# Kernel optimization log

Measured on AMD Instinct MI355X. Metric: run time of the kernel, lower is better.

The kernel has to match this reference:

```python
import jax, jax.numpy as jnp
import numpy as np

H = 12     # attention heads
W1S = 256  # one-sided sliding window (attention_window = 512)
NW = 8     # n_windows -> global tokens at each window start


def ln(x, g, b, eps=1e-5):
    m = jnp.mean(x, -1, keepdims=True)
    v = jnp.mean(jnp.square(x - m), -1, keepdims=True)
    return (x - m) * jax.lax.rsqrt(v + eps) * g + b


def _forward(x, x_mask, word_emb, pos_emb, emb_g, emb_b, Wq, bq, Wk, bk, Wv, bv, Wo, bo,
             Wqg, bqg, Wkg, bkg, Wvg, bvg, ln1_g, ln1_b, W1, b1, W2, b2, ln2_g, ln2_b,
             out_w, out_b):
    B, S = x.shape
    D = word_emb.shape[1]
    Dh = D // H
    w = W1S
    nb = S // w
    win_len = S // NW
    g = NW
    gpos = jnp.arange(g) * win_len
    scale = 1.0 / np.sqrt(Dh)

    x_mask = x_mask.at[:, gpos].set(1)  # module forces global slots to be valid
    kmask = x_mask > 0
    is_glob = jnp.zeros((S,), bool).at[gpos].set(True)

    h = ln(word_emb[x] + pos_emb[None], emb_g, emb_b)

    # static masks for the banded (sliding-window) scores
    kidx = jnp.arange(nb)[:, None] * w + jnp.arange(3 * w)[None, :] - w  # [nb,3w] abs key idx
    in_rng = (kidx >= 0) & (kidx < S)
    kidx_c = jnp.clip(kidx, 0, S - 1)
    key_ok = in_rng[None] & kmask[:, kidx_c] & (~is_glob[kidx_c])[None]   # [B,nb,3w]
    diff = jnp.arange(3 * w)[None, :] - w - jnp.arange(w)[:, None]        # [w,3w] key-query offset
    band_mask = ((jnp.abs(diff) <= w)[None, None] & key_ok[:, :, None, :]).reshape(B, 1, S, 3 * w)
    gkey_mask = kmask[:, gpos][:, None, None, :]                           # [B,1,1,g]
    mask_all = jnp.concatenate([jnp.broadcast_to(gkey_mask, (B, 1, S, g)),
                                jnp.broadcast_to(band_mask, (B, 1, S, 3 * w))], -1)

    def heads(t):
        return t.reshape(B, S, H, Dh).transpose(0, 2, 1, 3)

    def chunk3(t):  # [B,H,S,Dh] -> [B,H,nb,3w,Dh]; block n covers key offsets [-w, 2w)
        tp = jnp.pad(t, ((0, 0), (0, 0), (w, w), (0, 0))).reshape(B, H, nb + 2, w, Dh)
        return jnp.concatenate([tp[:, :, :nb], tp[:, :, 1:nb + 1], tp[:, :, 2:]], axis=3)

    def layer(h, p):
        (wq, bq_, wk, bk_, wv, bv_, wo, bo_, wqg, bqg_, wkg, bkg_, wvg, bvg_,
         g1, gb1, w1, fb1, w2, fb2, g2, gb2) = p
        q = heads(h @ wq + bq_); k = heads(h @ wk + bk_); v = heads(h @ wv + bv_)
        # sliding-window band scores + extra global-key columns, joint softmax
        sb = jnp.einsum('bhnqd,bhnkd->bhnqk', q.reshape(B, H, nb, w, Dh), chunk3(k)) * scale
        sg = jnp.einsum('bhsd,bhgd->bhsg', q, k[:, :, gpos]) * scale
        scores = jnp.concatenate([sg, sb.reshape(B, H, S, 3 * w)], -1)
        neg = jnp.finfo(scores.dtype).min * 0.5
        probs = jax.nn.softmax(jnp.where(mask_all, scores, neg), -1)
        ctx = (jnp.einsum('bhnqk,bhnkd->bhnqd', probs[..., g:].reshape(B, H, nb, w, 3 * w), chunk3(v)).reshape(B, H, S, Dh)
               + jnp.einsum('bhsg,bhgd->bhsd', probs[..., :g], v[:, :, gpos]))
        ctx = ctx.transpose(0, 2, 1, 3).reshape(B, S, D)
        # global-token queries: full attention over all keys with separate projections
        qg = (h[:, gpos] @ wqg + bqg_).reshape(B, g, H, Dh).transpose(0, 2, 1, 3)
        kg = heads(h @ wkg + bkg_); vg = heads(h @ wvg + bvg_)
        sgl = jnp.where(kmask[:, None, None, :], jnp.einsum('bhgd,bhsd->bhgs', qg, kg) * scale, neg)
        ctxg = jnp.einsum('bhgs,bhsd->bhgd', jax.nn.softmax(sgl, -1), vg).transpose(0, 2, 1, 3).reshape(B, g, D)
        ctx = ctx.at[:, gpos].set(ctxg)
        h = ln(h + ctx @ wo + bo_, g1, gb1)
        h = ln(h + jax.nn.gelu(h @ w1 + fb1, approximate=False) @ w2 + fb2, g2, gb2)
        return h, None

    params = (Wq, bq, Wk, bk, Wv, bv, Wo, bo, Wqg, bqg, Wkg, bkg, Wvg, bvg,
              ln1_g, ln1_b, W1, b1, W2, b2, ln2_g, ln2_b)
    h, _ = jax.lax.scan(jax.checkpoint(layer), h, params)
    y = h.reshape(B * NW, win_len, D)[:, 0]   # CLS pooling per window
    return y @ out_w + out_b


def setup_inputs():
    key = jax.random.key(0)
    V, S, D, L, F, O, B = 50265, 4096, 768, 12, 3072, 128, 1
    ks = iter(jax.random.split(key, 40))
    def nrm(shape):
        return (jax.random.normal(next(ks), shape) * 0.02).astype(jnp.float32)
    inp = {
        'x': jax.random.randint(next(ks), (B, S), 0, V, dtype=jnp.int32),
        'x_mask': jnp.ones((B, S), jnp.int32),
        'word_emb': nrm((V, D)), 'pos_emb': nrm((S, D)),
        'emb_g': jnp.ones((D,)), 'emb_b': jnp.zeros((D,)),
        'Wq': nrm((L, D, D)), 'bq': jnp.zeros((L, D)),
        'Wk': nrm((L, D, D)), 'bk': jnp.zeros((L, D)),
        'Wv': nrm((L, D, D)), 'bv': jnp.zeros((L, D)),
        'Wo': nrm((L, D, D)), 'bo': jnp.zeros((L, D)),
        'Wqg': nrm((L, D, D)), 'bqg': jnp.zeros((L, D)),
        'Wkg': nrm((L, D, D)), 'bkg': jnp.zeros((L, D)),
        'Wvg': nrm((L, D, D)), 'bvg': jnp.zeros((L, D)),
        'ln1_g': jnp.ones((L, D)), 'ln1_b': jnp.zeros((L, D)),
        'W1': nrm((L, D, F)), 'b1': jnp.zeros((L, F)),
        'W2': nrm((L, F, D)), 'b2': jnp.zeros((L, D)),
        'ln2_g': jnp.ones((L, D)), 'ln2_b': jnp.zeros((L, D)),
        'out_w': nrm((D, O)), 'out_b': jnp.zeros((O,)),
    }
    return inp


def reference(x, x_mask, word_emb, pos_emb, emb_g, emb_b, Wq, bq, Wk, bk, Wv, bv, Wo, bo,
              Wqg, bqg, Wkg, bkg, Wvg, bvg, ln1_g, ln1_b, W1, b1, W2, b2, ln2_g, ln2_b,
              out_w, out_b):
    return _forward(x, x_mask, word_emb, pos_emb, emb_g, emb_b, Wq, bq, Wk, bk, Wv, bv,
                    Wo, bo, Wqg, bqg, Wkg, bkg, Wvg, bvg, ln1_g, ln1_b, W1, b1, W2, b2,
                    ln2_g, ln2_b, out_w, out_b)
```

## Files before the change

### kernel.cpp

```cpp
#include <hip/hip_runtime.h>
#include <cstddef>

#define S_LEN   4096
#define DMODEL  768
#define NHEAD   12
#define DHEAD   64
#define FDIM    3072
#define NLAYER  12
#define WIN     256
#define NGLOB   8
#define GSTRIDE 512

typedef short bf16x8 __attribute__((ext_vector_type(8)));
typedef float f32x4 __attribute__((ext_vector_type(4)));
typedef unsigned short u16;

__device__ __forceinline__ u16 f2bf(float f) {
  unsigned u = __builtin_bit_cast(unsigned, f);
  return (u16)((u + 0x7FFFu + ((u >> 16) & 1u)) >> 16);
}
__device__ __forceinline__ float bf2f(u16 s) {
  unsigned u = ((unsigned)s) << 16;
  return __builtin_bit_cast(float, u);
}

__device__ __forceinline__ void gload16(const void* g, void* l) {
  __builtin_amdgcn_global_load_lds(
      (const __attribute__((address_space(1))) void*)g,
      (__attribute__((address_space(3))) void*)l, 16, 0, 0);
}

__device__ __forceinline__ float wave_sum(float v) {
#pragma unroll
  for (int off = 32; off > 0; off >>= 1) v += __shfl_xor(v, off);
  return v;
}

__device__ __forceinline__ float block_sum256(float v, float* sbuf) {
  v = wave_sum(v);
  int w = threadIdx.x >> 6;
  __syncthreads();
  if ((threadIdx.x & 63) == 0) sbuf[w] = v;
  __syncthreads();
  return sbuf[0] + sbuf[1] + sbuf[2] + sbuf[3];
}

__global__ __launch_bounds__(256) void embed_ln_kernel(
    const int* __restrict__ x, const float* __restrict__ wemb,
    const float* __restrict__ pemb, const float* __restrict__ gg,
    const float* __restrict__ bb, float* __restrict__ h, u16* __restrict__ hb) {
  __shared__ float sbuf[4];
  int s = blockIdx.x, tid = threadIdx.x;
  int idx = x[s];
  float vals[3];
#pragma unroll
  for (int i = 0; i < 3; i++) {
    int d = tid + i * 256;
    vals[i] = wemb[(size_t)idx * DMODEL + d] + pemb[(size_t)s * DMODEL + d];
  }
  float mean = block_sum256(vals[0] + vals[1] + vals[2], sbuf) * (1.0f / 768.0f);
  float sq = 0.f;
#pragma unroll
  for (int i = 0; i < 3; i++) { float t = vals[i] - mean; sq += t * t; }
  float inv = rsqrtf(block_sum256(sq, sbuf) * (1.0f / 768.0f) + 1e-5f);
#pragma unroll
  for (int i = 0; i < 3; i++) {
    int d = tid + i * 256;
    float r = (vals[i] - mean) * inv * gg[d] + bb[d];
    h[(size_t)s * DMODEL + d] = r;
    hb[(size_t)s * DMODEL + d] = f2bf(r);
  }
}

__global__ __launch_bounds__(256) void add_ln_kernel(
    float* __restrict__ h, const float* __restrict__ r,
    const float* __restrict__ gg, const float* __restrict__ bb,
    u16* __restrict__ hb) {
  __shared__ float sbuf[4];
  int s = blockIdx.x, tid = threadIdx.x;
  float vals[3];
#pragma unroll
  for (int i = 0; i < 3; i++) {
    int d = tid + i * 256;
    vals[i] = h[(size_t)s * DMODEL + d] + r[(size_t)s * DMODEL + d];
  }
  float mean = block_sum256(vals[0] + vals[1] + vals[2], sbuf) * (1.0f / 768.0f);
  float sq = 0.f;
#pragma unroll
  for (int i = 0; i < 3; i++) { float t = vals[i] - mean; sq += t * t; }
  float inv = rsqrtf(block_sum256(sq, sbuf) * (1.0f / 768.0f) + 1e-5f);
#pragma unroll
  for (int i = 0; i < 3; i++) {
    int d = tid + i * 256;
    float rr = (vals[i] - mean) * inv * gg[d] + bb[d];
    h[(size_t)s * DMODEL + d] = rr;
    hb[(size_t)s * DMODEL + d] = f2bf(rr);
  }
}

#define DD_ ((size_t)DMODEL * DMODEL)
#define DF_ ((size_t)DMODEL * FDIM)
#define WSTRIDE (6 * DD_ + 2 * DF_)
__global__ __launch_bounds__(256) void convw_kernel(
    const float* __restrict__ Wq, const float* __restrict__ Wk,
    const float* __restrict__ Wv, const float* __restrict__ Wkg,
    const float* __restrict__ Wvg, const float* __restrict__ Wo,
    const float* __restrict__ W1, const float* __restrict__ W2,
    u16* __restrict__ wt) {
  int l = blockIdx.y;
  int bid = blockIdx.x;
  const float* src; u16* dst; int K, N, r;
  u16* base = wt + (size_t)l * WSTRIDE;
  if (bid < 864) {
    int m = bid / 144; r = bid % 144; K = 768; N = 768;
    switch (m) {
      case 0: src = Wq  + l * DD_; dst = base;           break;
      case 1: src = Wk  + l * DD_; dst = base + 1 * DD_; break;
      case 2: src = Wv  + l * DD_; dst = base + 2 * DD_; break;
      case 3: src = Wkg + l * DD_; dst = base + 3 * DD_; break;
      case 4: src = Wvg + l * DD_; dst = base + 4 * DD_; break;
      default: src = Wo + l * DD_; dst = base + 5 * DD_; break;
    }
  } else if (bid < 1440) {
    r = bid - 864; K = 768; N = 3072; src = W1 + l * DF_; dst = base + 6 * DD_;
  } else {
    r = bid - 1440; K = 3072; N = 768; src = W2 + l * DF_; dst = base + 6 * DD_ + DF_;
  }
  int nt = N / 64;
  int tk = (r / nt) * 64, tn = (r % nt) * 64;
  int t = threadIdx.x;
  int c = t >> 2, ko = t & 3;
#pragma unroll
  for (int p = 0; p < 2; p++) {
    int kb = (p * 4 + ko) * 8;
    const float* sp = src + (size_t)(tk + kb) * N + tn + c;
    bf16x8 val;
#pragma unroll
    for (int j = 0; j < 8; j++) val[j] = (short)f2bf(sp[(size_t)j * N]);
    *(bf16x8*)&dst[(size_t)(tn + c) * K + tk + kb] = val;
  }
}

template <int ACT, int OUTM, int TM>
__device__ __forceinline__ void mm_core(const u16* __restrict__ A, const u16* __restrict__ Wt,
                                        const float* __restrict__ bias, void* __restrict__ Cv,
                                        int M, int N, int K, int bm, int bn,
                                        u16* As, u16* Bs) {
  constexpr int MR = TM / 32;
  constexpr int AJ = TM / 32;
  int t = threadIdx.x;
  int wid = t >> 6, lane = t & 63;
  int wr = (wid >> 1) * (TM / 2), wc = (wid & 1) * 64;
  int lr = lane & 15, lg = lane >> 4;
  f32x4 acc[MR][4];
  f32x4 zf = {0.f, 0.f, 0.f, 0.f};
#pragma unroll
  for (int m = 0; m < MR; m++)
#pragma unroll
    for (int n = 0; n < 4; n++) acc[m][n] = zf;

  int srow = wid * 8 + (lane >> 3);
  int sgr = (lane & 7) ^ (lane >> 3);
  const u16* aSrc = A + (size_t)(bm + srow) * K + sgr * 8;
  const u16* bSrc = Wt + (size_t)(bn + srow) * K + sgr * 8;
  int dstOff = wid * 8 * 64;

  for (int kt = 0; kt < K; kt += 64) {
    __syncthreads();
#pragma unroll
    for (int j = 0; j < AJ; j++)
      gload16(aSrc + kt + (size_t)j * 32 * K, As + dstOff + j * 32 * 64);
#pragma unroll
    for (int j = 0; j < 4; j++)
      gload16(bSrc + kt + (size_t)j * 32 * K, Bs + dstOff + j * 32 * 64);
    __syncthreads();
#pragma unroll
    for (int ks = 0; ks < 2; ks++) {
      bf16x8 af[MR], bfr[4];
#pragma unroll
      for (int m = 0; m < MR; m++)
        af[m] = *(const bf16x8*)&As[(wr + m * 16 + lr) * 64 + (((ks * 4 + lg) ^ (lr & 7)) * 8)];
#pragma unroll
      for (int n = 0; n < 4; n++)
        bfr[n] = *(const bf16x8*)&Bs[(wc + n * 16 + lr) * 64 + (((ks * 4 + lg) ^ (lr & 7)) * 8)];
#pragma unroll
      for (int m = 0; m < MR; m++)
#pragma unroll
        for (int n = 0; n < 4; n++)
          acc[m][n] = __builtin_amdgcn_mfma_f32_16x16x32_bf16(af[m], bfr[n], acc[m][n], 0, 0, 0);
    }
  }
#pragma unroll
  for (int n = 0; n < 4; n++) {
    int col = bn + wc + n * 16 + lr;
    float bb = bias[col];
#pragma unroll
    for (int m = 0; m < MR; m++) {
#pragma unroll
      for (int r = 0; r < 4; r++) {
        int row = bm + wr + m * 16 + lg * 4 + r;
        float xv = acc[m][n][r] + bb;
        if (ACT == 1) xv = 0.5f * xv * (1.0f + erff(xv * 0.70710678118654752f));
        if (OUTM == 0) ((float*)Cv)[(size_t)row * N + col] = xv;
        else if (OUTM == 1) ((u16*)Cv)[(size_t)row * N + col] = f2bf(xv);
        else ((u16*)Cv)[(size_t)col * M + row] = f2bf(xv);
      }
    }
  }
}

template <int ACT, int OUTM, int TM>
__global__ __launch_bounds__(256) void mm_kernel(const u16* A, const u16* Wt, const float* bias,
                                                 void* Cv, int M, int N, int K) {
  __shared__ u16 As[TM * 64];
  __shared__ u16 Bs[128 * 64];
  mm_core<ACT, OUTM, TM>(A, Wt, bias, Cv, M, N, K, blockIdx.y * TM, blockIdx.x * 128, As, Bs);
}

__global__ __launch_bounds__(256) void mm5_kernel(
    const u16* A,
    const u16* W0, const u16* W1_, const u16* W2_, const u16* W3, const u16* W4,
    const float* b0, const float* b1, const float* b2, const float* b3, const float* b4,
    u16* C0, u16* C1, u16* C2, u16* C3, u16* C4, int M, int K,
    const float* __restrict__ h, const float* __restrict__ Wqg,
    const float* __restrict__ bqg, float* __restrict__ qg) {
  __shared__ u16 As[128 * 64];
  __shared__ u16 Bs[128 * 64];
  if (blockIdx.x == 30) {
    int b = blockIdx.y;
    if (b >= 24) return;
    int gi = b / 3, c0 = (b % 3) * 256;
    int tid = threadIdx.x;
    float* hs = (float*)As;
    const float* hrow = h + (size_t)gi * GSTRIDE * DMODEL;
    for (int i = tid; i < DMODEL; i += 256) hs[i] = hrow[i];
    __syncthreads();
    float a = bqg[c0 + tid];
    for (int k = 0; k < DMODEL; k++) a += hs[k] * Wqg[(size_t)k * DMODEL + c0 + tid];
    qg[gi * DMODEL + c0 + tid] = a;
    return;
  }
  int which = blockIdx.x / 6;
  int bn = (blockIdx.x % 6) * 128;
  const u16* Ws[5] = {W0, W1_, W2_, W3, W4};
  const float* bs[5] = {b0, b1, b2, b3, b4};
  u16* Cs[5] = {C0, C1, C2, C3, C4};
  if (which == 2 || which == 4)
    mm_core<0, 2, 128>(A, Ws[which], bs[which], Cs[which], M, DMODEL, K, blockIdx.y * 128, bn, As, Bs);
  else
    mm_core<0, 1, 128>(A, Ws[which], bs[which], Cs[which], M, DMODEL, K, blockIdx.y * 128, bn, As, Bs);
}

__device__ __forceinline__ void sliding_body(
    int bid, u16* Ps,
    const u16* __restrict__ qb, const u16* __restrict__ kb,
    const u16* __restrict__ vt, const int* __restrict__ xmask,
    u16* __restrict__ ctx) {
  int hh = bid >> 6;
  int q0 = (bid & 63) * 64;
  int w = threadIdx.x >> 6, lane = threadIdx.x & 63;
  int lr = lane & 15, lg = lane >> 4;
  f32x4 zf = {0.f, 0.f, 0.f, 0.f};

  const u16* qptr = qb + (size_t)(q0 + w * 16 + lr) * DMODEL + hh * DHEAD;
  bf16x8 qf0 = *(const bf16x8*)(qptr + lg * 8);
  bf16x8 qf1 = *(const bf16x8*)(qptr + 32 + lg * 8);

  float m_run[4] = {-1e30f, -1e30f, -1e30f, -1e30f};
  float l_run[4] = {0.f, 0.f, 0.f, 0.f};
  f32x4 ctxa[4] = {zf, zf, zf, zf};

  {
    int krow = (lr < NGLOB) ? lr * GSTRIDE : 0;
    const u16* kp = kb + (size_t)krow * DMODEL + hh * DHEAD + lg * 8;
    f32x4 sa = __builtin_amdgcn_mfma_f32_16x16x32_bf16(qf0, *(const bf16x8*)kp, zf, 0, 0, 0);
    sa = __builtin_amdgcn_mfma_f32_16x16x32_bf16(qf1, *(const bf16x8*)(kp + 32), sa, 0, 0, 0);
    float p0[4], tmax[4];
#pragma unroll
    for (int r = 0; r < 4; r++) {
      float s = (lr < NGLOB) ? sa[r] * 0.125f : -1e30f;
      p0[r] = s; tmax[r] = s;
    }
#pragma unroll
    for (int o = 8; o; o >>= 1)
#pragma unroll
      for (int r = 0; r < 4; r++) tmax[r] = fmaxf(tmax[r], __shfl_xor(tmax[r], o));
    float tsum[4];
#pragma unroll
    for (int r = 0; r < 4; r++) {
      float mn = fmaxf(m_run[r], tmax[r]);
      m_run[r] = mn;
      p0[r] = __expf(p0[r] - mn);
      tsum[r] = p0[r];
    }
#pragma unroll
    for (int o = 8; o; o >>= 1)
#pragma unroll
      for (int r = 0; r < 4; r++) tsum[r] += __shfl_xor(tsum[r], o);
#pragma unroll
    for (int r = 0; r < 4; r++) l_run[r] = tsum[r];
#pragma unroll
    for (int r = 0; r < 4; r++) {
      int qi = lg * 4 + r;
      Ps[w * 1024 + qi * 64 + (((lr >> 3) ^ (qi & 7)) * 8) + (lr & 7)] = f2bf(p0[r]);
      int k2 = 16 + lr;
      Ps[w * 1024 + qi * 64 + (((k2 >> 3) ^ (qi & 7)) * 8) + (k2 & 7)] = 0;
    }
    bf16x8 pf = *(const bf16x8*)&Ps[w * 1024 + lr * 64 + ((lg ^ (lr & 7)) * 8)];
#pragma unroll
    for (int c2 = 0; c2 < 4; c2++) {
      bf16x8 vg8 = {0, 0, 0, 0, 0, 0, 0, 0};
      if (lg == 0) {
        const u16* vrow = vt + (size_t)(hh * DHEAD + c2 * 16 + lr) * S_LEN;
#pragma unroll
        for (int j = 0; j < 8; j++) vg8[j] = (short)vrow[(size_t)j * GSTRIDE];
      }
      ctxa[c2] = __builtin_amdgcn_mfma_f32_16x16x32_bf16(pf, vg8, ctxa[c2], 0, 0, 0);
    }
  }

  for (int tt = 0; tt < 9; tt++) {
    int base = q0 - WIN + tt * 64;
    if (base + 63 < 0 || base >= S_LEN) continue;
    f32x4 sa[4];
    int keyc[4]; bool vc[4];
#pragma unroll
    for (int c = 0; c < 4; c++) {
      int key = base + c * 16 + lr;
      int krow = key < 0 ? 0 : (key > S_LEN - 1 ? S_LEN - 1 : key);
      vc[c] = (key >= 0) && (key < S_LEN) && ((key & (GSTRIDE - 1)) != 0) && (xmask[krow] != 0);
      keyc[c] = key;
      const u16* kp = kb + (size_t)krow * DMODEL + hh * DHEAD + lg * 8;
      sa[c] = __builtin_amdgcn_mfma_f32_16x16x32_bf16(qf0, *(const bf16x8*)kp, zf, 0, 0, 0);
      sa[c] = __builtin_amdgcn_mfma_f32_16x16x32_bf16(qf1, *(const bf16x8*)(kp + 32), sa[c], 0, 0, 0);
    }
    float p[4][4], tmax[4] = {-1e30f, -1e30f, -1e30f, -1e30f};
#pragma unroll
    for (int c = 0; c < 4; c++)
#pragma unroll
      for (int r = 0; r < 4; r++) {
        int qrow = q0 + w * 16 + lg * 4 + r;
        int dd = keyc[c] - qrow;
        float s = (vc[c] && dd >= -WIN && dd <= WIN) ? sa[c][r] * 0.125f : -1e30f;
        p[c][r] = s;
        tmax[r] = fmaxf(tmax[r], s);
      }
#pragma unroll
    for (int o = 8; o; o >>= 1)
#pragma unroll
      for (int r = 0; r < 4; r++) tmax[r] = fmaxf(tmax[r], __shfl_xor(tmax[r], o));
    float sc[4], tsum[4] = {0.f, 0.f, 0.f, 0.f};
#pragma unroll
    for (int r = 0; r < 4; r++) {
      float mn = fmaxf(m_run[r], tmax[r]);
      sc[r] = __expf(m_run[r] - mn);
      m_run[r] = mn;
    }
#pragma unroll
    for (int c = 0; c < 4; c++)
#pragma unroll
      for (int r = 0; r < 4; r++) {
        p[c][r] = __expf(p[c][r] - m_run[r]);
        tsum[r] += p[c][r];
      }
#pragma unroll
    for (int o = 8; o; o >>= 1)
#pragma unroll
      for (int r = 0; r < 4; r++) tsum[r] += __shfl_xor(tsum[r], o);
#pragma unroll
    for (int r = 0; r < 4; r++) l_run[r] = l_run[r] * sc[r] + tsum[r];
#pragma unroll
    for (int c2 = 0; c2 < 4; c2++)
#pragma unroll
      for (int r = 0; r < 4; r++) ctxa[c2][r] *= sc[r];
#pragma unroll
    for (int c = 0; c < 4; c++)
#pragma unroll
      for (int r = 0; r < 4; r++) {
        int qi = lg * 4 + r, k64 = c * 16 + lr;
        Ps[w * 1024 + qi * 64 + (((k64 >> 3) ^ (qi & 7)) * 8) + (k64 & 7)] = f2bf(p[c][r]);
      }
#pragma unroll
    for (int ks = 0; ks < 2; ks++) {
      bf16x8 pf = *(const bf16x8*)&Ps[w * 1024 + lr * 64 + (((ks * 4 + lg) ^ (lr & 7)) * 8)];
      int kstart = base + ks * 32 + lg * 8;
      int kc = kstart < 0 ? 0 : (kstart > S_LEN - 8 ? S_LEN - 8 : kstart);
#pragma unroll
      for (int c2 = 0; c2 < 4; c2++) {
        const u16* vp = vt + (size_t)(hh * DHEAD + c2 * 16 + lr) * S_LEN + kc;
        ctxa[c2] = __builtin_amdgcn_mfma_f32_16x16x32_bf16(pf, *(const bf16x8*)vp, ctxa[c2], 0, 0, 0);
      }
    }
  }

#pragma unroll
  for (int c2 = 0; c2 < 4; c2++)
#pragma unroll
    for (int r = 0; r < 4; r++) {
      int qrow = q0 + w * 16 + lg * 4 + r;
      ctx[(size_t)qrow * DMODEL + hh * DHEAD + c2 * 16 + lr] = f2bf(ctxa[c2][r] / l_run[r]);
    }
}

__device__ __forceinline__ void gattn_body(
    int hh, int c, u16* Ps,
    const float* __restrict__ qg, const u16* __restrict__ kg,
    const u16* __restrict__ vgt, const int* __restrict__ xmask,
    float* __restrict__ pm, float* __restrict__ pl, float* __restrict__ pacc) {
  int w = threadIdx.x >> 6, lane = threadIdx.x & 63;
  int lr = lane & 15, lg = lane >> 4;
  int base = c * 256 + w * 64;
  f32x4 zf = {0.f, 0.f, 0.f, 0.f};

  bf16x8 qf0, qf1;
  {
    const float* qp = qg + (size_t)(lr & 7) * DMODEL + hh * DHEAD;
    bool real = lr < 8;
#pragma unroll
    for (int j = 0; j < 8; j++) {
      qf0[j] = real ? (short)f2bf(0.125f * qp[lg * 8 + j]) : (short)0;
      qf1[j] = real ? (short)f2bf(0.125f * qp[32 + lg * 8 + j]) : (short)0;
    }
  }

  f32x4 sa[4];
  bool vc[4];
#pragma unroll
  for (int st = 0; st < 4; st++) {
    int key = base + st * 16 + lr;
    vc[st] = (xmask[key] != 0) || ((key & (GSTRIDE - 1)) == 0);
    const u16* kp = kg + (size_t)key * DMODEL + hh * DHEAD + lg * 8;
    sa[st] = __builtin_amdgcn_mfma_f32_16x16x32_bf16(qf0, *(const bf16x8*)kp, zf, 0, 0, 0);
    sa[st] = __builtin_amdgcn_mfma_f32_16x16x32_bf16(qf1, *(const bf16x8*)(kp + 32), sa[st], 0, 0, 0);
  }
  float p[4][4], tmax[4] = {-1e30f, -1e30f, -1e30f, -1e30f};
#pragma unroll
  for (int st = 0; st < 4; st++)
#pragma unroll
    for (int r = 0; r < 4; r++) {
      float s = vc[st] ? sa[st][r] : -1e30f;
      p[st][r] = s;
      tmax[r] = fmaxf(tmax[r], s);
    }
#pragma unroll
  for (int o = 8; o; o >>= 1)
#pragma unroll
    for (int r = 0; r < 4; r++) tmax[r] = fmaxf(tmax[r], __shfl_xor(tmax[r], o));
  float tsum[4] = {0.f, 0.f, 0.f, 0.f};
#pragma unroll
  for (int st = 0; st < 4; st++)
#pragma unroll
    for (int r = 0; r < 4; r++) {
      float pv = vc[st] ? __expf(p[st][r] - tmax[r]) : 0.f;
      p[st][r] = pv;
      tsum[r] += pv;
    }
#pragma unroll
  for (int o = 8; o; o >>= 1)
#pragma unroll
    for (int r = 0; r < 4; r++) tsum[r] += __shfl_xor(tsum[r], o);
#pragma unroll
  for (int st = 0; st < 4; st++)
#pragma unroll
    for (int r = 0; r < 4; r++) {
      int qi = lg * 4 + r, k64 = st * 16 + lr;
      Ps[w * 1024 + qi * 64 + (((k64 >> 3) ^ (qi & 7)) * 8) + (k64 & 7)] = f2bf(p[st][r]);
    }
  f32x4 ctxa[4] = {zf, zf, zf, zf};
#pragma unroll
  for (int ks = 0; ks < 2; ks++) {
    bf16x8 pf = *(const bf16x8*)&Ps[w * 1024 + lr * 64 + (((ks * 4 + lg) ^ (lr & 7)) * 8)];
    int kstart = base + ks * 32 + lg * 8;
#pragma unroll
    for (int c2 = 0; c2 < 4; c2++) {
      const u16* vp = vgt + (size_t)(hh * DHEAD + c2 * 16 + lr) * S_LEN + kstart;
      ctxa[c2] = __builtin_amdgcn_mfma_f32_16x16x32_bf16(pf, *(const bf16x8*)vp, ctxa[c2], 0, 0, 0);
    }
  }
  int pidx = (hh * 16 + c) * 4 + w;
  if (lg < 2) {
#pragma unroll
    for (int r = 0; r < 4; r++) {
      int q = lg * 4 + r;
#pragma unroll
      for (int c2 = 0; c2 < 4; c2++)
        pacc[(size_t)pidx * 512 + q * 64 + c2 * 16 + lr] = ctxa[c2][r];
      if (lr == 0) {
        pm[pidx * 8 + q] = tmax[r];
        pl[pidx * 8 + q] = tsum[r];
      }
    }
  }
}

__global__ __launch_bounds__(256) void attn_kernel(
    const u16* __restrict__ qb, const u16* __restrict__ kb,
    const u16* __restrict__ vt, const int* __restrict__ xmask,
    u16* __restrict__ ctx,
    const float* __restrict__ qg, const u16* __restrict__ kg,
    const u16* __restrict__ vgt,
    float* __restrict__ pm, float* __restrict__ pl, float* __restrict__ pacc) {
  __shared__ u16 Ps[4 * 16 * 64];
  int bid = blockIdx.x;
  if (bid < NHEAD * 64) {
    sliding_body(bid, Ps, qb, kb, vt, xmask, ctx);
  } else {
    int idx = bid - NHEAD * 64;
    gattn_body(idx >> 4, idx & 15, Ps, qg, kg, vgt, xmask, pm, pl, pacc);
  }
}

__global__ __launch_bounds__(64) void gattn_comb_kernel(
    const float* __restrict__ pm, const float* __restrict__ pl,
    const float* __restrict__ pacc, u16* __restrict__ ctx) {
  int gi = blockIdx.x / NHEAD, hh = blockIdx.x % NHEAD;
  int d = threadIdx.x;
  float M = -1e30f, L = 0.f, A = 0.f;
  for (int i = 0; i < 64; i++) {
    int pidx = hh * 64 + i;
    float m_i = pm[pidx * 8 + gi];
    float l_i = pl[pidx * 8 + gi];
    float a_i = pacc[(size_t)pidx * 512 + gi * 64 + d];
    if (m_i > M) {
      float sc = __expf(M - m_i);
      A = A * sc + a_i;
      L = L * sc + l_i;
      M = m_i;
    } else {
      float sc = __expf(m_i - M);
      A += a_i * sc;
      L += l_i * sc;
    }
  }
  ctx[(size_t)gi * GSTRIDE * DMODEL + hh * DHEAD + d] = f2bf(A / L);
}

__global__ __launch_bounds__(128) void cls_out_kernel(
    const float* __restrict__ h, const float* __restrict__ ow,
    const float* __restrict__ ob, float* __restrict__ y) {
  __shared__ float hs[DMODEL];
  int wi = blockIdx.x;
  int tid = threadIdx.x;
  for (int i = tid; i < DMODEL; i += 128) hs[i] = h[(size_t)wi * GSTRIDE * DMODEL + i];
  __syncthreads();
  float a = ob[tid];
  for (int d = 0; d < DMODEL; d++) a += hs[d] * ow[d * 128 + tid];
  y[wi * 128 + tid] = a;
}

extern "C" void kernel_launch(void* const* d_in, const int* in_sizes, int n_in,
                              void* d_out, int out_size, void* d_ws, size_t ws_size,
                              hipStream_t stream) {
  const int*   x      = (const int*)d_in[0];
  const int*   xmask  = (const int*)d_in[1];
  const float* wemb   = (const float*)d_in[2];
  const float* pemb   = (const float*)d_in[3];
  const float* emb_g  = (const float*)d_in[4];
  const float* emb_b  = (const float*)d_in[5];
  const float* Wq     = (const float*)d_in[6];
  const float* bq     = (const float*)d_in[7];
  const float* Wk     = (const float*)d_in[8];
  const float* bk     = (const float*)d_in[9];
  const float* Wv     = (const float*)d_in[10];
  const float* bv     = (const float*)d_in[11];
  const float* Wo     = (const float*)d_in[12];
  const float* bo     = (const float*)d_in[13];
  const float* Wqg    = (const float*)d_in[14];
  const float* bqg    = (const float*)d_in[15];
  const float* Wkg    = (const float*)d_in[16];
  const float* bkg    = (const float*)d_in[17];
  const float* Wvg    = (const float*)d_in[18];
  const float* bvg    = (const float*)d_in[19];
  const float* ln1_g  = (const float*)d_in[20];
  const float* ln1_b  = (const float*)d_in[21];
  const float* W1     = (const float*)d_in[22];
  const float* b1     = (const float*)d_in[23];
  const float* W2     = (const float*)d_in[24];
  const float* b2     = (const float*)d_in[25];
  const float* ln2_g  = (const float*)d_in[26];
  const float* ln2_b  = (const float*)d_in[27];
  const float* out_w  = (const float*)d_in[28];
  const float* out_b  = (const float*)d_in[29];

  char* wsp = (char*)d_ws;
  float* h   = (float*)wsp;  wsp += (size_t)S_LEN * DMODEL * 4;
  float* tmp = (float*)wsp;  wsp += (size_t)S_LEN * DMODEL * 4;
  u16* hb  = (u16*)wsp;      wsp += (size_t)S_LEN * DMODEL * 2;
  u16* ctx = (u16*)wsp;      wsp += (size_t)S_LEN * DMODEL * 2;
  u16* qb  = (u16*)wsp;      wsp += (size_t)S_LEN * DMODEL * 2;
  u16* kb  = (u16*)wsp;      wsp += (size_t)S_LEN * DMODEL * 2;
  u16* vt  = (u16*)wsp;      wsp += (size_t)S_LEN * DMODEL * 2;
  u16* kgb = (u16*)wsp;      wsp += (size_t)S_LEN * DMODEL * 2;
  u16* vgt = (u16*)wsp;      wsp += (size_t)S_LEN * DMODEL * 2;
  u16* mid = (u16*)wsp;      wsp += (size_t)S_LEN * FDIM * 2;
  float* qgb = (float*)wsp;  wsp += (size_t)NGLOB * DMODEL * 4;
  float* pm = (float*)wsp;   wsp += (size_t)768 * 8 * 4;
  float* pl = (float*)wsp;   wsp += (size_t)768 * 8 * 4;
  float* pacc = (float*)wsp; wsp += (size_t)768 * 512 * 4;
  u16* wtb = (u16*)wsp;      wsp += WSTRIDE * NLAYER * 2;

  embed_ln_kernel<<<S_LEN, 256, 0, stream>>>(x, wemb, pemb, emb_g, emb_b, h, hb);
  convw_kernel<<<dim3(2016, NLAYER), 256, 0, stream>>>(Wq, Wk, Wv, Wkg, Wvg, Wo, W1, W2, wtb);

  for (int l = 0; l < NLAYER; l++) {
    const float* bql  = bq  + (size_t)l * DMODEL;
    const float* bkl  = bk  + (size_t)l * DMODEL;
    const float* bvl  = bv  + (size_t)l * DMODEL;
    const float* bol  = bo  + (size_t)l * DMODEL;
    const float* wqg  = Wqg + (size_t)l * DD_;
    const float* bqgl = bqg + (size_t)l * DMODEL;
    const float* bkgl = bkg + (size_t)l * DMODEL;
    const float* bvgl = bvg + (size_t)l * DMODEL;
    const float* b1l  = b1  + (size_t)l * FDIM;
    const float* b2l  = b2  + (size_t)l * DMODEL;
    u16* base = wtb + (size_t)l * WSTRIDE;
    u16* wqT  = base;
    u16* wkT  = base + 1 * DD_;
    u16* wvT  = base + 2 * DD_;
    u16* wkgT = base + 3 * DD_;
    u16* wvgT = base + 4 * DD_;
    u16* woT  = base + 5 * DD_;
    u16* w1T  = base + 6 * DD_;
    u16* w2T  = base + 6 * DD_ + DF_;

    mm5_kernel<<<dim3(31, 32), 256, 0, stream>>>(
        hb, wqT, wkT, wvT, wkgT, wvgT, bql, bkl, bvl, bkgl, bvgl,
        qb, kb, vt, kgb, vgt, S_LEN, DMODEL, h, wqg, bqgl, qgb);

    attn_kernel<<<NHEAD * 64 + NHEAD * 16, 256, 0, stream>>>(
        qb, kb, vt, xmask, ctx, qgb, kgb, vgt, pm, pl, pacc);
    gattn_comb_kernel<<<NGLOB * NHEAD, 64, 0, stream>>>(pm, pl, pacc, ctx);

    mm_kernel<0, 0, 64><<<dim3(6, 64), 256, 0, stream>>>(ctx, woT, bol, tmp, S_LEN, DMODEL, DMODEL);
    add_ln_kernel<<<S_LEN, 256, 0, stream>>>(h, tmp, ln1_g + (size_t)l * DMODEL,
                                             ln1_b + (size_t)l * DMODEL, hb);

    mm_kernel<1, 1, 128><<<dim3(24, 32), 256, 0, stream>>>(hb, w1T, b1l, mid, S_LEN, FDIM, DMODEL);
    mm_kernel<0, 0, 64><<<dim3(6, 64), 256, 0, stream>>>(mid, w2T, b2l, tmp, S_LEN, DMODEL, FDIM);
    add_ln_kernel<<<S_LEN, 256, 0, stream>>>(h, tmp, ln2_g + (size_t)l * DMODEL,
                                             ln2_b + (size_t)l * DMODEL, hb);
  }

  cls_out_kernel<<<NGLOB, 128, 0, stream>>>(h, out_w, out_b, (float*)d_out);
}
```

Baseline: 3.273 ms.

## Process two query fragments per wave in sliding-window attention to reuse K/V loads

Each sliding-window block now covers 128 query rows instead of 64, and each wave handles two 16-row query fragments that share the same K and V fragment loads. This halves the number of sliding blocks and the global K/V traffic per query. In exchange it raises register use, doubles the shared P buffer, and runs 10 key tiles per block instead of 9. It also lowers parallelism, since there are fewer blocks.

```diff
diff --git a/kernel.cpp b/kernel.cpp
--- a/kernel.cpp
+++ b/kernel.cpp
@@ -256,57 +256,73 @@
     const u16* __restrict__ qb, const u16* __restrict__ kb,
     const u16* __restrict__ vt, const int* __restrict__ xmask,
     u16* __restrict__ ctx) {
-  int hh = bid >> 6;
-  int q0 = (bid & 63) * 64;
+  int hh = bid >> 5;
+  int q0 = (bid & 31) * 128;
   int w = threadIdx.x >> 6, lane = threadIdx.x & 63;
   int lr = lane & 15, lg = lane >> 4;
+  int rowb = q0 + w * 32;
   f32x4 zf = {0.f, 0.f, 0.f, 0.f};
-
-  const u16* qptr = qb + (size_t)(q0 + w * 16 + lr) * DMODEL + hh * DHEAD;
-  bf16x8 qf0 = *(const bf16x8*)(qptr + lg * 8);
-  bf16x8 qf1 = *(const bf16x8*)(qptr + 32 + lg * 8);
-
-  float m_run[4] = {-1e30f, -1e30f, -1e30f, -1e30f};
-  float l_run[4] = {0.f, 0.f, 0.f, 0.f};
-  f32x4 ctxa[4] = {zf, zf, zf, zf};
+  u16* Pw = Ps + w * 2048;
+
+  bf16x8 qf[2][2];
+#pragma unroll
+  for (int mf = 0; mf < 2; mf++) {
+    const u16* qptr = qb + (size_t)(rowb + mf * 16 + lr) * DMODEL + hh * DHEAD;
+    qf[mf][0] = *(const bf16x8*)(qptr + lg * 8);
+    qf[mf][1] = *(const bf16x8*)(qptr + 32 + lg * 8);
+  }
+
+  float m_run[2][4], l_run[2][4];
+  f32x4 ctxa[2][4];
+#pragma unroll
+  for (int mf = 0; mf < 2; mf++)
+#pragma unroll
+    for (int r = 0; r < 4; r++) {
+      m_run[mf][r] = -1e30f; l_run[mf][r] = 0.f; ctxa[mf][r] = zf;
+    }
 
   {
     int krow = (lr < NGLOB) ? lr * GSTRIDE : 0;
     const u16* kp = kb + (size_t)krow * DMODEL + hh * DHEAD + lg * 8;
-    f32x4 sa = __builtin_amdgcn_mfma_f32_16x16x32_bf16(qf0, *(const bf16x8*)kp, zf, 0, 0, 0);
-    sa = __builtin_amdgcn_mfma_f32_16x16x32_bf16(qf1, *(const bf16x8*)(kp + 32), sa, 0, 0, 0);
-    float p0[4], tmax[4];
-#pragma unroll
-    for (int r = 0; r < 4; r++) {
-      float s = (lr < NGLOB) ? sa[r] * 0.125f : -1e30f;
-      p0[r] = s; tmax[r] = s;
-    }
-#pragma unroll
-    for (int o = 8; o; o >>= 1)
-#pragma unroll
-      for (int r = 0; r < 4; r++) tmax[r] = fmaxf(tmax[r], __shfl_xor(tmax[r], o));
-    float tsum[4];
-#pragma unroll
-    for (int r = 0; r < 4; r++) {
-      float mn = fmaxf(m_run[r], tmax[r]);
-      m_run[r] = mn;
-      p0[r] = __expf(p0[r] - mn);
-      tsum[r] = p0[r];
-    }
-#pragma unroll
-    for (int o = 8; o; o >>= 1)
-#pragma unroll
-      for (int r = 0; r < 4; r++) tsum[r] += __shfl_xor(tsum[r], o);
-#pragma unroll
-    for (int r = 0; r < 4; r++) l_run[r] = tsum[r];
-#pragma unroll
-    for (int r = 0; r < 4; r++) {
-      int qi = lg * 4 + r;
-      Ps[w * 1024 + qi * 64 + (((lr >> 3) ^ (qi & 7)) * 8) + (lr & 7)] = f2bf(p0[r]);
-      int k2 = 16 + lr;
-      Ps[w * 1024 + qi * 64 + (((k2 >> 3) ^ (qi & 7)) * 8) + (k2 & 7)] = 0;
-    }
-    bf16x8 pf = *(const bf16x8*)&Ps[w * 1024 + lr * 64 + ((lg ^ (lr & 7)) * 8)];
+    bf16x8 kf0 = *(const bf16x8*)kp;
+    bf16x8 kf1 = *(const bf16x8*)(kp + 32);
+#pragma unroll
+    for (int mf = 0; mf < 2; mf++) {
+      f32x4 sa = __builtin_amdgcn_mfma_f32_16x16x32_bf16(qf[mf][0], kf0, zf, 0, 0, 0);
+      sa = __builtin_amdgcn_mfma_f32_16x16x32_bf16(qf[mf][1], kf1, sa, 0, 0, 0);
+      float p0[4], tmax[4];
+#pragma unroll
+      for (int r = 0; r < 4; r++) {
+        float s = (lr < NGLOB) ? sa[r] * 0.125f : -1e30f;
+        p0[r] = s; tmax[r] = s;
+      }
+#pragma unroll
+      for (int o = 8; o; o >>= 1)
+#pragma unroll
+        for (int r = 0; r < 4; r++) tmax[r] = fmaxf(tmax[r], __shfl_xor(tmax[r], o));
+      float tsum[4];
+#pragma unroll
+      for (int r = 0; r < 4; r++) {
+        m_run[mf][r] = tmax[r];
+        p0[r] = __expf(p0[r] - tmax[r]);
+        tsum[r] = p0[r];
+      }
+#pragma unroll
+      for (int o = 8; o; o >>= 1)
+#pragma unroll
+        for (int r = 0; r < 4; r++) tsum[r] += __shfl_xor(tsum[r], o);
+#pragma unroll
+      for (int r = 0; r < 4; r++) l_run[mf][r] = tsum[r];
+#pragma unroll
+      for (int r = 0; r < 4; r++) {
+        int qi = mf * 16 + lg * 4 + r;
+        Pw[qi * 64 + (((lr >> 3) ^ (qi & 7)) * 8) + (lr & 7)] = f2bf(p0[r]);
+        int k2 = 16 + lr;
+        Pw[qi * 64 + (((k2 >> 3) ^ (qi & 7)) * 8) + (k2 & 7)] = 0;
+      }
+    }
+    bf16x8 pf0 = *(const bf16x8*)&Pw[lr * 64 + ((lg ^ (lr & 7)) * 8)];
+    bf16x8 pf1 = *(const bf16x8*)&Pw[(16 + lr) * 64 + ((lg ^ (lr & 7)) * 8)];
 #pragma unroll
     for (int c2 = 0; c2 < 4; c2++) {
       bf16x8 vg8 = {0, 0, 0, 0, 0, 0, 0, 0};
@@ -315,14 +331,15 @@
 #pragma unroll
         for (int j = 0; j < 8; j++) vg8[j] = (short)vrow[(size_t)j * GSTRIDE];
       }
-      ctxa[c2] = __builtin_amdgcn_mfma_f32_16x16x32_bf16(pf, vg8, ctxa[c2], 0, 0, 0);
-    }
-  }
-
-  for (int tt = 0; tt < 9; tt++) {
+      ctxa[0][c2] = __builtin_amdgcn_mfma_f32_16x16x32_bf16(pf0, vg8, ctxa[0][c2], 0, 0, 0);
+      ctxa[1][c2] = __builtin_amdgcn_mfma_f32_16x16x32_bf16(pf1, vg8, ctxa[1][c2], 0, 0, 0);
+    }
+  }
+
+  for (int tt = 0; tt < 10; tt++) {
     int base = q0 - WIN + tt * 64;
     if (base + 63 < 0 || base >= S_LEN) continue;
-    f32x4 sa[4];
+    bf16x8 kf[4][2];
     int keyc[4]; bool vc[4];
 #pragma unroll
     for (int c = 0; c < 4; c++) {
@@ -331,75 +348,89 @@
       vc[c] = (key >= 0) && (key < S_LEN) && ((key & (GSTRIDE - 1)) != 0) && (xmask[krow] != 0);
       keyc[c] = key;
       const u16* kp = kb + (size_t)krow * DMODEL + hh * DHEAD + lg * 8;
-      sa[c] = __builtin_amdgcn_mfma_f32_16x16x32_bf16(qf0, *(const bf16x8*)kp, zf, 0, 0, 0);
-      sa[c] = __builtin_amdgcn_mfma_f32_16x16x32_bf16(qf1, *(const bf16x8*)(kp + 32), sa[c], 0, 0, 0);
-    }
-    float p[4][4], tmax[4] = {-1e30f, -1e30f, -1e30f, -1e30f};
-#pragma unroll
-    for (int c = 0; c < 4; c++)
+      kf[c][0] = *(const bf16x8*)kp;
+      kf[c][1] = *(const bf16x8*)(kp + 32);
+    }
+#pragma unroll
+    for (int mf = 0; mf < 2; mf++) {
+      f32x4 sa[4];
+#pragma unroll
+      for (int c = 0; c < 4; c++) {
+        sa[c] = __builtin_amdgcn_mfma_f32_16x16x32_bf16(qf[mf][0], kf[c][0], zf, 0, 0, 0);
+        sa[c] = __builtin_amdgcn_mfma_f32_16x16x32_bf16(qf[mf][1], kf[c][1], sa[c], 0, 0, 0);
+      }
+      float p[4][4], tmax[4] = {-1e30f, -1e30f, -1e30f, -1e30f};
+#pragma unroll
+      for (int c = 0; c < 4; c++)
+#pragma unroll
+        for (int r = 0; r < 4; r++) {
+          int qrow = rowb + mf * 16 + lg * 4 + r;
+          int dd = keyc[c] - qrow;
+          float s = (vc[c] && dd >= -WIN && dd <= WIN) ? sa[c][r] * 0.125f : -1e30f;
+          p[c][r] = s;
+          tmax[r] = fmaxf(tmax[r], s);
+        }
+#pragma unroll
+      for (int o = 8; o; o >>= 1)
+#pragma unroll
+        for (int r = 0; r < 4; r++) tmax[r] = fmaxf(tmax[r], __shfl_xor(tmax[r], o));
+      float sc[4], tsum[4] = {0.f, 0.f, 0.f, 0.f};
 #pragma unroll
       for (int r = 0; r < 4; r++) {
-        int qrow = q0 + w * 16 + lg * 4 + r;
-        int dd = keyc[c] - qrow;
-        float s = (vc[c] && dd >= -WIN && dd <= WIN) ? sa[c][r] * 0.125f : -1e30f;
-        p[c][r] = s;
-        tmax[r] = fmaxf(tmax[r], s);
-      }
-#pragma unroll
-    for (int o = 8; o; o >>= 1)
-#pragma unroll
-      for (int r = 0; r < 4; r++) tmax[r] = fmaxf(tmax[r], __shfl_xor(tmax[r], o));
-    float sc[4], tsum[4] = {0.f, 0.f, 0.f, 0.f};
-#pragma unroll
-    for (int r = 0; r < 4; r++) {
-      float mn = fmaxf(m_run[r], tmax[r]);
-      sc[r] = __expf(m_run[r] - mn);
-      m_run[r] = mn;
-    }
-#pragma unroll
-    for (int c = 0; c < 4; c++)
-#pragma unroll
-      for (int r = 0; r < 4; r++) {
-        p[c][r] = __expf(p[c][r] - m_run[r]);
-        tsum[r] += p[c][r];
-      }
-#pragma unroll
-    for (int o = 8; o; o >>= 1)
-#pragma unroll
-      for (int r = 0; r < 4; r++) tsum[r] += __shfl_xor(tsum[r], o);
-#pragma unroll
-    for (int r = 0; r < 4; r++) l_run[r] = l_run[r] * sc[r] + tsum[r];
-#pragma unroll
-    for (int c2 = 0; c2 < 4; c2++)
-#pragma unroll
-      for (int r = 0; r < 4; r++) ctxa[c2][r] *= sc[r];
-#pragma unroll
-    for (int c = 0; c < 4; c++)
-#pragma unroll
-      for (int r = 0; r < 4; r++) {
-        int qi = lg * 4 + r, k64 = c * 16 + lr;
-        Ps[w * 1024 + qi * 64 + (((k64 >> 3) ^ (qi & 7)) * 8) + (k64 & 7)] = f2bf(p[c][r]);
-      }
+        float mn = fmaxf(m_run[mf][r], tmax[r]);
+        sc[r] = __expf(m_run[mf][r] - mn);
+        m_run[mf][r] = mn;
+      }
+#pragma unroll
+      for (int c = 0; c < 4; c++)
+#pragma unroll
+        for (int r = 0; r < 4; r++) {
+          p[c][r] = __expf(p[c][r] - m_run[mf][r]);
+          tsum[r] += p[c][r];
+        }
+#pragma unroll
+      for (int o = 8; o; o >>= 1)
+#pragma unroll
+        for (int r = 0; r < 4; r++) tsum[r] += __shfl_xor(tsum[r], o);
+#pragma unroll
+      for (int r = 0; r < 4; r++) l_run[mf][r] = l_run[mf][r] * sc[r] + tsum[r];
+#pragma unroll
+      for (int c2 = 0; c2 < 4; c2++)
+#pragma unroll
+        for (int r = 0; r < 4; r++) ctxa[mf][c2][r] *= sc[r];
+#pragma unroll
+      for (int c = 0; c < 4; c++)
+#pragma unroll
+        for (int r = 0; r < 4; r++) {
+          int qi = mf * 16 + lg * 4 + r, k64 = c * 16 + lr;
+          Pw[qi * 64 + (((k64 >> 3) ^ (qi & 7)) * 8) + (k64 & 7)] = f2bf(p[c][r]);
+        }
+    }
 #pragma unroll
     for (int ks = 0; ks < 2; ks++) {
-      bf16x8 pf = *(const bf16x8*)&Ps[w * 1024 + lr * 64 + (((ks * 4 + lg) ^ (lr & 7)) * 8)];
+      bf16x8 pf0 = *(const bf16x8*)&Pw[lr * 64 + (((ks * 4 + lg) ^ (lr & 7)) * 8)];
+      bf16x8 pf1 = *(const bf16x8*)&Pw[(16 + lr) * 64 + (((ks * 4 + lg) ^ (lr & 7)) * 8)];
       int kstart = base + ks * 32 + lg * 8;
       int kc = kstart < 0 ? 0 : (kstart > S_LEN - 8 ? S_LEN - 8 : kstart);
 #pragma unroll
       for (int c2 = 0; c2 < 4; c2++) {
         const u16* vp = vt + (size_t)(hh * DHEAD + c2 * 16 + lr) * S_LEN + kc;
-        ctxa[c2] = __builtin_amdgcn_mfma_f32_16x16x32_bf16(pf, *(const bf16x8*)vp, ctxa[c2], 0, 0, 0);
-      }
-    }
-  }
-
-#pragma unroll
-  for (int c2 = 0; c2 < 4; c2++)
-#pragma unroll
-    for (int r = 0; r < 4; r++) {
-      int qrow = q0 + w * 16 + lg * 4 + r;
-      ctx[(size_t)qrow * DMODEL + hh * DHEAD + c2 * 16 + lr] = f2bf(ctxa[c2][r] / l_run[r]);
-    }
+        bf16x8 vf = *(const bf16x8*)vp;
+        ctxa[0][c2] = __builtin_amdgcn_mfma_f32_16x16x32_bf16(pf0, vf, ctxa[0][c2], 0, 0, 0);
+        ctxa[1][c2] = __builtin_amdgcn_mfma_f32_16x16x32_bf16(pf1, vf, ctxa[1][c2], 0, 0, 0);
+      }
+    }
+  }
+
+#pragma unroll
+  for (int mf = 0; mf < 2; mf++)
+#pragma unroll
+    for (int c2 = 0; c2 < 4; c2++)
+#pragma unroll
+      for (int r = 0; r < 4; r++) {
+        int qrow = rowb + mf * 16 + lg * 4 + r;
+        ctx[(size_t)qrow * DMODEL + hh * DHEAD + c2 * 16 + lr] = f2bf(ctxa[mf][c2][r] / l_run[mf][r]);
+      }
 }
 
 __device__ __forceinline__ void gattn_body(
@@ -500,12 +531,12 @@
     const float* __restrict__ qg, const u16* __restrict__ kg,
     const u16* __restrict__ vgt,
     float* __restrict__ pm, float* __restrict__ pl, float* __restrict__ pacc) {
-  __shared__ u16 Ps[4 * 16 * 64];
+  __shared__ u16 Ps[4 * 32 * 64];
   int bid = blockIdx.x;
-  if (bid < NHEAD * 64) {
+  if (bid < NHEAD * 32) {
     sliding_body(bid, Ps, qb, kb, vt, xmask, ctx);
   } else {
-    int idx = bid - NHEAD * 64;
+    int idx = bid - NHEAD * 32;
     gattn_body(idx >> 4, idx & 15, Ps, qg, kg, vgt, xmask, pm, pl, pacc);
   }
 }
@@ -627,7 +658,7 @@
         hb, wqT, wkT, wvT, wkgT, wvgT, bql, bkl, bvl, bkgl, bvgl,
         qb, kb, vt, kgb, vgt, S_LEN, DMODEL, h, wqg, bqgl, qgb);
 
-    attn_kernel<<<NHEAD * 64 + NHEAD * 16, 256, 0, stream>>>(
+    attn_kernel<<<NHEAD * 32 + NHEAD * 16, 256, 0, stream>>>(
         qb, kb, vt, xmask, ctx, qgb, kgb, vgt, pm, pl, pacc);
     gattn_comb_kernel<<<NGLOB * NHEAD, 64, 0, stream>>>(pm, pl, pacc, ctx);
 
```

After: 3.130 ms. 4.4% less time.
